# Optimization experiments

Hardware: AMD Instinct MI355X
Metric: run time of the kernel (lower is better)

The kernel has to match this reference:

```python
import jax, jax.numpy as jnp
import numpy as np

B, T = 32, 8192
RNN, ENC, ATT, LOC, K = 1024, 512, 128, 32, 31


def setup_inputs() -> dict:
    key = jax.random.key(0)
    ks = jax.random.split(key, 9)
    return {
        'queries': jax.random.normal(ks[0], (B, RNN), jnp.float32),
        'memories': jax.random.normal(ks[1], (B, ENC, T), jnp.float32),
        'processed_memories': jax.random.normal(ks[2], (B, ATT, T), jnp.float32),
        'previous_alignments': jax.random.uniform(ks[3], (B, T), jnp.float32),
        'cumulated_alignments': jax.random.uniform(ks[4], (B, T), jnp.float32),
        'masks': jnp.zeros((B, T), jnp.bool_),
        # learned params (xavier-ish scale)
        'w_query': jax.random.normal(ks[5], (ATT, RNN), jnp.float32) * (1.0 / np.sqrt(RNN)),
        'w_loc_conv': jax.random.normal(ks[6], (LOC, 2, K), jnp.float32) * (1.0 / np.sqrt(2 * K)),
        'w_loc_1x1': jax.random.normal(ks[7], (ATT, LOC), jnp.float32) * (1.0 / np.sqrt(LOC)),
        'w_score': jax.random.normal(ks[8], (ATT,), jnp.float32) * (1.0 / np.sqrt(ATT)),
    }


def reference(queries, memories, processed_memories, previous_alignments,
              cumulated_alignments, masks, w_query, w_loc_conv, w_loc_1x1, w_score):
    # ---- Calc_Score ----
    # Query 1x1 conv == matmul: [B, ATT, 1]
    q = (queries @ w_query.T)[:, :, None]
    # Location features: conv over [B, 2, T] (same padding), then 1x1 -> [B, ATT, T]
    attn_cat = jnp.stack([previous_alignments, cumulated_alignments], axis=1)  # [B,2,T]
    pad = (K - 1) // 2
    loc = jax.lax.conv_general_dilated(attn_cat, w_loc_conv, (1,), [(pad, pad)],
                                       dimension_numbers=('NCH', 'OIH', 'NCH'))  # [B,LOC,T]
    loc = jnp.einsum('blt,al->bat', loc, w_loc_1x1)  # [B,ATT,T]
    scores = jnp.einsum('bat,a->bt', jnp.tanh(q + processed_memories + loc), w_score)  # [B,T]
    # ---- Apply_Score (sigmoid_noise = 0) ----
    scores = jnp.where(masks, -jnp.finfo(scores.dtype).max, scores)
    p = jax.nn.sigmoid(scores)  # p_choose_i, [B,T]
    # stepwise monotonic update: a_t = prev*p + shift_right(prev*(1-p))
    shifted = jnp.pad((previous_alignments * (1.0 - p))[:, :-1], ((0, 0), (1, 0)))
    alignments = previous_alignments * p + shifted  # [B,T]
    contexts = jnp.einsum('bt,bct->bc', alignments, memories)  # [B,ENC]
    return contexts, alignments
```

## Files before the change

### kernel.cpp

```cpp
#include <hip/hip_runtime.h>
#include <math.h>

#define B_   32
#define T_   8192
#define RNN_ 1024
#define ENC_ 512
#define ATT_ 128
#define LOC_ 32
#define K_   31
#define PAD_ 15

typedef __fp16 half2v __attribute__((ext_vector_type(2)));

__device__ __forceinline__ float fdot2(unsigned int a, unsigned int b, float c) {
    return __builtin_amdgcn_fdot2(__builtin_bit_cast(half2v, a),
                                  __builtin_bit_cast(half2v, b), c, false);
}

__device__ __forceinline__ unsigned int packh2(float x, float y) {
    half2v h;
    h.x = (__fp16)x;
    h.y = (__fp16)y;
    return __builtin_bit_cast(unsigned int, h);
}

__device__ __forceinline__ float fast_tanh(float x) {
    x = fminf(15.f, fmaxf(-15.f, x));
    float e = __expf(2.f * x);
    return (e - 1.f) * __builtin_amdgcn_rcpf(e + 1.f);
}

__device__ __forceinline__ float fast_sigmoid(float x) {
    x = fminf(30.f, fmaxf(-30.f, x));
    float e = __expf(-x);
    return __builtin_amdgcn_rcpf(1.f + e);
}

__global__ __launch_bounds__(256) void k_prep_query(const float* __restrict__ queries,
                                                    const float* __restrict__ wq,
                                                    const float* __restrict__ wconv,
                                                    const float* __restrict__ w1,
                                                    float* __restrict__ qout,
                                                    unsigned int* __restrict__ wTh2,
                                                    unsigned int* __restrict__ w1h2) {
    if (blockIdx.x == (B_ * ATT_) / 4) {
        for (int i = threadIdx.x; i < K_ * LOC_; i += blockDim.x) {
            int k = i / LOC_;
            int l = i % LOC_;
            float wp = wconv[l * (2 * K_) + k];
            float wc = wconv[l * (2 * K_) + K_ + k];
            wTh2[i] = packh2(wp, wc);
        }
        for (int i = threadIdx.x; i < ATT_ * (LOC_ / 2); i += blockDim.x) {
            int a = i / (LOC_ / 2);
            int p = i % (LOC_ / 2);
            w1h2[i] = packh2(w1[a * LOC_ + 2 * p], w1[a * LOC_ + 2 * p + 1]);
        }
        return;
    }
    int w    = blockIdx.x * 4 + (threadIdx.x >> 6);
    int lane = threadIdx.x & 63;
    int b = w >> 7, a = w & 127;
    const float4* qrow = (const float4*)(queries + (size_t)b * RNN_);
    const float4* wrow = (const float4*)(wq + (size_t)a * RNN_);
    float acc = 0.f;
#pragma unroll
    for (int i = 0; i < 4; ++i) {
        float4 x = qrow[i * 64 + lane];
        float4 y = wrow[i * 64 + lane];
        acc += x.x * y.x + x.y * y.y + x.z * y.z + x.w * y.w;
    }
#pragma unroll
    for (int off = 32; off; off >>= 1) acc += __shfl_xor(acc, off);
    if (lane == 0) qout[b * ATT_ + a] = acc;
}

#define BLK2  256
#define TILE2 256

__global__ __launch_bounds__(256) void k_score(
    const float* __restrict__ pm,
    const float* __restrict__ prev,
    const float* __restrict__ cum,
    const unsigned char* __restrict__ masks,
    const float* __restrict__ qbuf,
    const unsigned int* __restrict__ wTh2,
    const unsigned int* __restrict__ w1h2,
    const float* __restrict__ wsc,
    float* __restrict__ pout)
{
    __shared__ unsigned int sPC[TILE2 + K_ - 1];
    int blk  = blockIdx.x;
    int b    = blk >> 5;
    int tile = blk & 31;
    int tbase = tile * TILE2;
    const float* prow = prev + (size_t)b * T_;
    const float* crow = cum + (size_t)b * T_;
    for (int i = threadIdx.x; i < TILE2 + K_ - 1; i += BLK2) {
        int g = tbase - PAD_ + i;
        bool ok = (g >= 0) && (g < T_);
        float pv = ok ? prow[g] : 0.f;
        float cv = ok ? crow[g] : 0.f;
        sPC[i] = packh2(pv, cv);
    }
    __syncthreads();

    int lt = threadIdx.x;
    int t0 = tbase + lt;

    float loc[LOC_];
#pragma unroll
    for (int l = 0; l < LOC_; ++l) loc[l] = 0.f;

    for (int k = 0; k < K_; ++k) {
        unsigned int pc = sPC[lt + k];
        const uint4* wk4 = (const uint4*)(wTh2 + k * LOC_);
#pragma unroll
        for (int lq = 0; lq < 8; ++lq) {
            uint4 wv = wk4[lq];
            loc[4 * lq + 0] = fdot2(wv.x, pc, loc[4 * lq + 0]);
            loc[4 * lq + 1] = fdot2(wv.y, pc, loc[4 * lq + 1]);
            loc[4 * lq + 2] = fdot2(wv.z, pc, loc[4 * lq + 2]);
            loc[4 * lq + 3] = fdot2(wv.w, pc, loc[4 * lq + 3]);
        }
    }

    unsigned int lh[LOC_ / 2];
#pragma unroll
    for (int i = 0; i < LOC_ / 2; ++i)
        lh[i] = packh2(loc[2 * i], loc[2 * i + 1]);

    float score = 0.f;
    const float* pmb = pm + (size_t)b * ATT_ * T_ + t0;
    const float* qb  = qbuf + b * ATT_;
#pragma unroll 2
    for (int a = 0; a < ATT_; ++a) {
        float q   = qb[a];
        float wsa = wsc[a];
        const uint4* wa4 = (const uint4*)(w1h2 + a * (LOC_ / 2));
        float pmv = pmb[(size_t)a * T_];
        float l2a = 0.f, l2b = 0.f;
        uint4 w0 = wa4[0];
        uint4 w1v = wa4[1];
        uint4 w2 = wa4[2];
        uint4 w3 = wa4[3];
        l2a = fdot2(w0.x, lh[0],  l2a);  l2b = fdot2(w1v.x, lh[4],  l2b);
        l2a = fdot2(w0.y, lh[1],  l2a);  l2b = fdot2(w1v.y, lh[5],  l2b);
        l2a = fdot2(w0.z, lh[2],  l2a);  l2b = fdot2(w1v.z, lh[6],  l2b);
        l2a = fdot2(w0.w, lh[3],  l2a);  l2b = fdot2(w1v.w, lh[7],  l2b);
        l2a = fdot2(w2.x, lh[8],  l2a);  l2b = fdot2(w3.x, lh[12], l2b);
        l2a = fdot2(w2.y, lh[9],  l2a);  l2b = fdot2(w3.y, lh[13], l2b);
        l2a = fdot2(w2.z, lh[10], l2a);  l2b = fdot2(w3.z, lh[14], l2b);
        l2a = fdot2(w2.w, lh[11], l2a);  l2b = fdot2(w3.w, lh[15], l2b);
        score += wsa * fast_tanh(q + pmv + l2a + l2b);
    }

    unsigned char m = masks[(size_t)b * T_ + t0];
    float s = m ? -3.0e38f : score;
    pout[(size_t)b * T_ + t0] = fast_sigmoid(s);
}

__global__ __launch_bounds__(256) void k_align(const float* __restrict__ p,
                                               const float* __restrict__ prev,
                                               float* __restrict__ align) {
    int idx = blockIdx.x * blockDim.x + threadIdx.x;
    int b  = idx / (T_ / 4);
    int t0 = (idx % (T_ / 4)) * 4;
    const float* pr = p + (size_t)b * T_;
    const float* vr = prev + (size_t)b * T_;
    float4 p4 = *(const float4*)(pr + t0);
    float4 v4 = *(const float4*)(vr + t0);
    float pm1 = (t0 > 0) ? pr[t0 - 1] : 0.f;
    float vm1 = (t0 > 0) ? vr[t0 - 1] : 0.f;
    float4 o;
    o.x = v4.x * p4.x + vm1 * (1.f - pm1);
    o.y = v4.y * p4.y + v4.x * (1.f - p4.x);
    o.z = v4.z * p4.z + v4.y * (1.f - p4.y);
    o.w = v4.w * p4.w + v4.z * (1.f - p4.z);
    *(float4*)(align + (size_t)b * T_ + t0) = o;
}

__global__ __launch_bounds__(256) void k_context(const float* __restrict__ mem,
                                                 const float* __restrict__ align,
                                                 float* __restrict__ ctx) {
    int w    = blockIdx.x * 4 + (threadIdx.x >> 6);
    int lane = threadIdx.x & 63;
    int b = w >> 9;
    int c = w & 511;
    const float4* mrow = (const float4*)(mem + ((size_t)b * ENC_ + c) * T_);
    const float4* arow = (const float4*)(align + (size_t)b * T_);
    float acc0 = 0.f, acc1 = 0.f;
#pragma unroll 8
    for (int i = 0; i < T_ / 256; ++i) {
        float4 m = mrow[i * 64 + lane];
        float4 a = arow[i * 64 + lane];
        if (i & 1)
            acc1 += m.x * a.x + m.y * a.y + m.z * a.z + m.w * a.w;
        else
            acc0 += m.x * a.x + m.y * a.y + m.z * a.z + m.w * a.w;
    }
    float acc = acc0 + acc1;
#pragma unroll
    for (int off = 32; off; off >>= 1) acc += __shfl_xor(acc, off);
    if (lane == 0) ctx[b * ENC_ + c] = acc;
}

extern "C" void kernel_launch(void* const* d_in, const int* in_sizes, int n_in,
                              void* d_out, int out_size, void* d_ws, size_t ws_size,
                              hipStream_t stream) {
    const float* queries = (const float*)d_in[0];
    const float* memories = (const float*)d_in[1];
    const float* pm = (const float*)d_in[2];
    const float* prev = (const float*)d_in[3];
    const float* cum = (const float*)d_in[4];
    const unsigned char* masks = (const unsigned char*)d_in[5];
    const float* w_query = (const float*)d_in[6];
    const float* w_conv = (const float*)d_in[7];
    const float* w_1x1 = (const float*)d_in[8];
    const float* w_score = (const float*)d_in[9];

    float* out_ctx = (float*)d_out;
    float* out_align = (float*)d_out + (size_t)B_ * ENC_;

    float* ws_q = (float*)d_ws;
    float* ws_p = ws_q + B_ * ATT_;
    unsigned int* ws_wTh2 = (unsigned int*)(ws_p + (size_t)B_ * T_);
    unsigned int* ws_w1h2 = ws_wTh2 + K_ * LOC_ + 32;

    hipLaunchKernelGGL(k_prep_query, dim3((B_ * ATT_) / 4 + 1), dim3(256), 0, stream,
                       queries, w_query, w_conv, w_1x1, ws_q, ws_wTh2, ws_w1h2);
    hipLaunchKernelGGL(k_score, dim3(B_ * (T_ / TILE2)), dim3(BLK2), 0, stream,
                       pm, prev, cum, masks, ws_q, ws_wTh2, ws_w1h2, w_score, ws_p);
    hipLaunchKernelGGL(k_align, dim3((B_ * T_ / 4) / 256), dim3(256), 0, stream,
                       ws_p, prev, out_align);
    hipLaunchKernelGGL(k_context, dim3((B_ * ENC_) / 4), dim3(256), 0, stream,
                       memories, out_align, out_ctx);
}
```

Measured before the change: 167.9 us.

## Split score ATT reduction across four wavefronts with LDS-staged processed memories

The score kernel now handles 64 time steps per block instead of 256, and its four wavefronts each reduce a quarter of the ATT dimension. Partial scores are combined through shared memory. The processed_memories tile is staged into LDS with float4 loads, and the grid grows fourfold to give more blocks and better load coalescing. In exchange, each wavefront recomputes the full 31-tap location convolution, so that conv work is done four times over, and the kernel adds an extra barrier and about 32KB of LDS per block.

```diff
diff --git a/kernel.cpp b/kernel.cpp
--- a/kernel.cpp
+++ b/kernel.cpp
@@ -75,8 +75,8 @@
     if (lane == 0) qout[b * ATT_ + a] = acc;
 }
 
-#define BLK2  256
-#define TILE2 256
+#define BLK2 256
+#define TS2  64
 
 __global__ __launch_bounds__(256) void k_score(
     const float* __restrict__ pm,
@@ -89,29 +89,40 @@
     const float* __restrict__ wsc,
     float* __restrict__ pout)
 {
-    __shared__ unsigned int sPC[TILE2 + K_ - 1];
+    __shared__ float sPM[ATT_][TS2];
+    __shared__ unsigned int sPC[TS2 + K_ - 1];
+    __shared__ float sPart[TS2][4];
+
     int blk  = blockIdx.x;
-    int b    = blk >> 5;
-    int tile = blk & 31;
-    int tbase = tile * TILE2;
+    int b    = blk >> 7;
+    int tile = blk & 127;
+    int tbase = tile * TS2;
+    int tid = threadIdx.x;
+
+    const float* pmb = pm + (size_t)b * ATT_ * T_ + tbase;
+#pragma unroll
+    for (int rep = 0; rep < 8; ++rep) {
+        int idx = rep * BLK2 + tid;
+        int row = idx >> 4;
+        int c4  = idx & 15;
+        float4 v = *(const float4*)(pmb + (size_t)row * T_ + c4 * 4);
+        *(float4*)(&sPM[row][c4 * 4]) = v;
+    }
     const float* prow = prev + (size_t)b * T_;
     const float* crow = cum + (size_t)b * T_;
-    for (int i = threadIdx.x; i < TILE2 + K_ - 1; i += BLK2) {
+    for (int i = tid; i < TS2 + K_ - 1; i += BLK2) {
         int g = tbase - PAD_ + i;
         bool ok = (g >= 0) && (g < T_);
-        float pv = ok ? prow[g] : 0.f;
-        float cv = ok ? crow[g] : 0.f;
-        sPC[i] = packh2(pv, cv);
+        sPC[i] = packh2(ok ? prow[g] : 0.f, ok ? crow[g] : 0.f);
     }
     __syncthreads();
 
-    int lt = threadIdx.x;
-    int t0 = tbase + lt;
+    int lt = tid & 63;
+    int ag = tid >> 6;
 
     float loc[LOC_];
 #pragma unroll
     for (int l = 0; l < LOC_; ++l) loc[l] = 0.f;
-
     for (int k = 0; k < K_; ++k) {
         unsigned int pc = sPC[lt + k];
         const uint4* wk4 = (const uint4*)(wTh2 + k * LOC_);
@@ -124,21 +135,20 @@
             loc[4 * lq + 3] = fdot2(wv.w, pc, loc[4 * lq + 3]);
         }
     }
-
     unsigned int lh[LOC_ / 2];
 #pragma unroll
     for (int i = 0; i < LOC_ / 2; ++i)
         lh[i] = packh2(loc[2 * i], loc[2 * i + 1]);
 
     float score = 0.f;
-    const float* pmb = pm + (size_t)b * ATT_ * T_ + t0;
-    const float* qb  = qbuf + b * ATT_;
+    const float* qb = qbuf + b * ATT_;
 #pragma unroll 2
-    for (int a = 0; a < ATT_; ++a) {
+    for (int aa = 0; aa < 32; ++aa) {
+        int a = ag * 32 + aa;
         float q   = qb[a];
         float wsa = wsc[a];
         const uint4* wa4 = (const uint4*)(w1h2 + a * (LOC_ / 2));
-        float pmv = pmb[(size_t)a * T_];
+        float pmv = sPM[a][lt];
         float l2a = 0.f, l2b = 0.f;
         uint4 w0 = wa4[0];
         uint4 w1v = wa4[1];
@@ -154,10 +164,15 @@
         l2a = fdot2(w2.w, lh[11], l2a);  l2b = fdot2(w3.w, lh[15], l2b);
         score += wsa * fast_tanh(q + pmv + l2a + l2b);
     }
-
-    unsigned char m = masks[(size_t)b * T_ + t0];
-    float s = m ? -3.0e38f : score;
-    pout[(size_t)b * T_ + t0] = fast_sigmoid(s);
+    sPart[lt][ag] = score;
+    __syncthreads();
+
+    if (tid < TS2) {
+        float s = sPart[tid][0] + sPart[tid][1] + sPart[tid][2] + sPart[tid][3];
+        unsigned char m = masks[(size_t)b * T_ + tbase + tid];
+        float sc = m ? -3.0e38f : s;
+        pout[(size_t)b * T_ + tbase + tid] = fast_sigmoid(sc);
+    }
 }
 
 __global__ __launch_bounds__(256) void k_align(const float* __restrict__ p,
@@ -229,7 +244,7 @@
 
     hipLaunchKernelGGL(k_prep_query, dim3((B_ * ATT_) / 4 + 1), dim3(256), 0, stream,
                        queries, w_query, w_conv, w_1x1, ws_q, ws_wTh2, ws_w1h2);
-    hipLaunchKernelGGL(k_score, dim3(B_ * (T_ / TILE2)), dim3(BLK2), 0, stream,
+    hipLaunchKernelGGL(k_score, dim3(B_ * (T_ / TS2)), dim3(BLK2), 0, stream,
                        pm, prev, cum, masks, ws_q, ws_wTh2, ws_w1h2, w_score, ws_p);
     hipLaunchKernelGGL(k_align, dim3((B_ * T_ / 4) / 256), dim3(256), 0, stream,
                        ws_p, prev, out_align);
```

Measured after the change: 214.6 us. +27.9%, slower.

## Split score ATT reduction across two blocks and fuse sigmoid into align

Applied to the files above, without the earlier changes.

The score kernel now launches twice as many blocks, each handling half of the 128 attention channels and writing a partial score to a workspace buffer. The align kernel sums the two partials, applies the mask and sigmoid, then does the monotonic update. This is meant to raise occupancy and parallelism on the k_score stage, which previously had only 1024 blocks. The cost is that each block recomputes the location conv, and an extra partial buffer is written and read. A launch-bounds occupancy hint was also added.

```diff
diff --git a/kernel.cpp b/kernel.cpp
--- a/kernel.cpp
+++ b/kernel.cpp
@@ -78,30 +78,28 @@
 #define BLK2  256
 #define TILE2 256
 
-__global__ __launch_bounds__(256) void k_score(
+__global__ __launch_bounds__(256, 8) void k_score(
     const float* __restrict__ pm,
     const float* __restrict__ prev,
     const float* __restrict__ cum,
-    const unsigned char* __restrict__ masks,
     const float* __restrict__ qbuf,
     const unsigned int* __restrict__ wTh2,
     const unsigned int* __restrict__ w1h2,
     const float* __restrict__ wsc,
-    float* __restrict__ pout)
+    float* __restrict__ part)
 {
     __shared__ unsigned int sPC[TILE2 + K_ - 1];
     int blk  = blockIdx.x;
-    int b    = blk >> 5;
-    int tile = blk & 31;
+    int b    = blk >> 6;
+    int tile = (blk >> 1) & 31;
+    int ag   = blk & 1;
     int tbase = tile * TILE2;
     const float* prow = prev + (size_t)b * T_;
     const float* crow = cum + (size_t)b * T_;
     for (int i = threadIdx.x; i < TILE2 + K_ - 1; i += BLK2) {
         int g = tbase - PAD_ + i;
         bool ok = (g >= 0) && (g < T_);
-        float pv = ok ? prow[g] : 0.f;
-        float cv = ok ? crow[g] : 0.f;
-        sPC[i] = packh2(pv, cv);
+        sPC[i] = packh2(ok ? prow[g] : 0.f, ok ? crow[g] : 0.f);
     }
     __syncthreads();
 
@@ -131,14 +129,16 @@
         lh[i] = packh2(loc[2 * i], loc[2 * i + 1]);
 
     float score = 0.f;
-    const float* pmb = pm + (size_t)b * ATT_ * T_ + t0;
-    const float* qb  = qbuf + b * ATT_;
+    const float* pmb = pm + ((size_t)b * ATT_ + ag * 64) * T_ + t0;
+    const float* qb  = qbuf + b * ATT_ + ag * 64;
+    const float* wsb = wsc + ag * 64;
+    const unsigned int* w1b = w1h2 + (ag * 64) * (LOC_ / 2);
 #pragma unroll 2
-    for (int a = 0; a < ATT_; ++a) {
-        float q   = qb[a];
-        float wsa = wsc[a];
-        const uint4* wa4 = (const uint4*)(w1h2 + a * (LOC_ / 2));
-        float pmv = pmb[(size_t)a * T_];
+    for (int aa = 0; aa < 64; ++aa) {
+        float q   = qb[aa];
+        float wsa = wsb[aa];
+        const uint4* wa4 = (const uint4*)(w1b + aa * (LOC_ / 2));
+        float pmv = pmb[(size_t)aa * T_];
         float l2a = 0.f, l2b = 0.f;
         uint4 w0 = wa4[0];
         uint4 w1v = wa4[1];
@@ -155,23 +155,38 @@
         score += wsa * fast_tanh(q + pmv + l2a + l2b);
     }
 
-    unsigned char m = masks[(size_t)b * T_ + t0];
-    float s = m ? -3.0e38f : score;
-    pout[(size_t)b * T_ + t0] = fast_sigmoid(s);
-}
-
-__global__ __launch_bounds__(256) void k_align(const float* __restrict__ p,
+    part[(size_t)ag * B_ * T_ + (size_t)b * T_ + t0] = score;
+}
+
+__global__ __launch_bounds__(256) void k_align(const float* __restrict__ part,
+                                               const unsigned char* __restrict__ masks,
                                                const float* __restrict__ prev,
                                                float* __restrict__ align) {
     int idx = blockIdx.x * blockDim.x + threadIdx.x;
     int b  = idx / (T_ / 4);
     int t0 = (idx % (T_ / 4)) * 4;
-    const float* pr = p + (size_t)b * T_;
+    const float* p0 = part + (size_t)b * T_;
+    const float* p1 = part + (size_t)B_ * T_ + (size_t)b * T_;
     const float* vr = prev + (size_t)b * T_;
-    float4 p4 = *(const float4*)(pr + t0);
+    const unsigned char* mrow = masks + (size_t)b * T_;
+
+    float4 s0 = *(const float4*)(p0 + t0);
+    float4 s1 = *(const float4*)(p1 + t0);
     float4 v4 = *(const float4*)(vr + t0);
-    float pm1 = (t0 > 0) ? pr[t0 - 1] : 0.f;
-    float vm1 = (t0 > 0) ? vr[t0 - 1] : 0.f;
+    uchar4 m4 = *(const uchar4*)(mrow + t0);
+
+    float4 p4;
+    p4.x = m4.x ? 0.f : fast_sigmoid(s0.x + s1.x);
+    p4.y = m4.y ? 0.f : fast_sigmoid(s0.y + s1.y);
+    p4.z = m4.z ? 0.f : fast_sigmoid(s0.z + s1.z);
+    p4.w = m4.w ? 0.f : fast_sigmoid(s0.w + s1.w);
+
+    float pm1 = 0.f, vm1 = 0.f;
+    if (t0 > 0) {
+        unsigned char mprev = mrow[t0 - 1];
+        pm1 = mprev ? 0.f : fast_sigmoid(p0[t0 - 1] + p1[t0 - 1]);
+        vm1 = vr[t0 - 1];
+    }
     float4 o;
     o.x = v4.x * p4.x + vm1 * (1.f - pm1);
     o.y = v4.y * p4.y + v4.x * (1.f - p4.x);
@@ -223,16 +238,16 @@
     float* out_align = (float*)d_out + (size_t)B_ * ENC_;
 
     float* ws_q = (float*)d_ws;
-    float* ws_p = ws_q + B_ * ATT_;
-    unsigned int* ws_wTh2 = (unsigned int*)(ws_p + (size_t)B_ * T_);
+    float* ws_part = ws_q + B_ * ATT_;
+    unsigned int* ws_wTh2 = (unsigned int*)(ws_part + (size_t)2 * B_ * T_);
     unsigned int* ws_w1h2 = ws_wTh2 + K_ * LOC_ + 32;
 
     hipLaunchKernelGGL(k_prep_query, dim3((B_ * ATT_) / 4 + 1), dim3(256), 0, stream,
                        queries, w_query, w_conv, w_1x1, ws_q, ws_wTh2, ws_w1h2);
-    hipLaunchKernelGGL(k_score, dim3(B_ * (T_ / TILE2)), dim3(BLK2), 0, stream,
-                       pm, prev, cum, masks, ws_q, ws_wTh2, ws_w1h2, w_score, ws_p);
+    hipLaunchKernelGGL(k_score, dim3(B_ * 32 * 2), dim3(BLK2), 0, stream,
+                       pm, prev, cum, ws_q, ws_wTh2, ws_w1h2, w_score, ws_part);
     hipLaunchKernelGGL(k_align, dim3((B_ * T_ / 4) / 256), dim3(256), 0, stream,
-                       ws_p, prev, out_align);
+                       ws_part, masks, prev, out_align);
     hipLaunchKernelGGL(k_context, dim3((B_ * ENC_) / 4), dim3(256), 0, stream,
                        memories, out_align, out_ctx);
 }
```

Result: slower. 194.4 us (+15.8%).
